# Kernel optimization log

Measured on AMD Instinct MI355X. Metric: run time of the kernel, lower is better.

Reference implementation:

```python
import jax, jax.numpy as jnp
import numpy as np

B, H, W, D, L, M = 16, 256, 256, 32, 4, 12  # batch, grid H, grid W, d_model, num_layers, modes
BN_EPS = 1e-5


def setup_inputs() -> dict:
    key = jax.random.key(0)
    ks = jax.random.split(key, 12)
    scale = 1.0 / (D * D)  # SpectralConv2d init scale: 1/(in_ch*out_ch)
    return {
        "x": jax.random.normal(ks[0], (B, H, W), jnp.float32),
        "coords_x": jax.random.uniform(ks[1], (1, 2, 1, H, W), dtype=jnp.float32),
        # linear_in: 3 -> D
        "w_in": jax.random.normal(ks[2], (D, 3), jnp.float32) * 0.3,
        "b_in": jnp.zeros((D,), jnp.float32),
        # per-layer spectral weights (real/imag), torch.rand-style uniform [0,1)*scale
        "w1r": jax.random.uniform(ks[3], (L, D, D, M, M), dtype=jnp.float32) * scale,
        "w1i": jax.random.uniform(ks[4], (L, D, D, M, M), dtype=jnp.float32) * scale,
        "w2r": jax.random.uniform(ks[5], (L, D, D, M, M), dtype=jnp.float32) * scale,
        "w2i": jax.random.uniform(ks[6], (L, D, D, M, M), dtype=jnp.float32) * scale,
        # per-layer pointwise linear D -> D
        "lw": jax.random.normal(ks[7], (L, D, D), jnp.float32) * (1.0 / np.sqrt(D)),
        "lb": jnp.zeros((L, D), jnp.float32),
        # per-layer BatchNorm affine params
        "gamma": jnp.ones((L, D), jnp.float32),
        "beta": jnp.zeros((L, D), jnp.float32),
        # linear_out: D -> 1
        "w_out": jax.random.normal(ks[8], (1, D), jnp.float32) * (1.0 / np.sqrt(D)),
        "b_out": jnp.zeros((1,), jnp.float32),
    }


def _fourier_layer(h, w1, w2, lw, lb, gamma, beta):
    # h: [B, D, H, W]
    Bh, C, Hh, Wh = h.shape
    h_ft = jnp.fft.rfft2(h)  # [B, D, H, W//2+1] complex64
    # low-mode truncation + complex channel mixing on two corner blocks
    top = jnp.einsum('bixy,ioxy->boxy', h_ft[:, :, :M, :M], w1)
    bot = jnp.einsum('bixy,ioxy->boxy', h_ft[:, :, Hh - M:, :M], w2)
    out_ft = jnp.zeros((Bh, C, Hh, Wh // 2 + 1), jnp.complex64)
    out_ft = out_ft.at[:, :, :M, :M].set(top).at[:, :, Hh - M:, :M].set(bot)
    y = jnp.fft.irfft2(out_ft, s=(Hh, Wh))  # [B, D, H, W]
    # residual pointwise linear (x + Linear(x)), then ReLU, then BatchNorm2d (batch stats)
    y = y + jnp.einsum('bchw,oc->bohw', y, lw) + lb[None, :, None, None]
    y = jax.nn.relu(y)
    mean = y.mean(axis=(0, 2, 3), keepdims=True)
    var = y.var(axis=(0, 2, 3), keepdims=True)
    y = (y - mean) * jax.lax.rsqrt(var + BN_EPS)
    return y * gamma[None, :, None, None] + beta[None, :, None, None]


def reference(x, coords_x, w_in, b_in, w1r, w1i, w2r, w2i, lw, lb, gamma, beta, w_out, b_out):
    # coords_x: [1,2,1,H,W] -> squeeze dim 2 -> broadcast to [B,2,H,W]
    cx = jnp.broadcast_to(coords_x[:, :, 0], (x.shape[0], 2, H, W))
    h = jnp.concatenate([x[:, None], cx], axis=1)  # [B, 3, H, W]
    h = jnp.einsum('bchw,dc->bdhw', h, w_in) + b_in[None, :, None, None]  # linear_in
    for i in range(L):  # fixed small layer count
        h = _fourier_layer(h, w1r[i] + 1j * w1i[i], w2r[i] + 1j * w2i[i],
                           lw[i], lb[i], gamma[i], beta[i])
    out = jnp.einsum('bdhw,od->bohw', h, w_out) + b_out[None, :, None, None]  # linear_out
    return out[:, 0]  # [B, H, W]
```

## Files before the change

### kernel.cpp

```cpp
#include <hip/hip_runtime.h>

constexpr double PI2 = 6.283185307179586476925286766559;
constexpr float INV_HW = 1.0f / 65536.0f;


__global__ __launch_bounds__(256) void k_init(float* __restrict__ cs) {
  int t = threadIdx.x;
  double a = PI2 * (double)t / 256.0;
  cs[2*t]   = (float)cos(a);
  cs[2*t+1] = (float)sin(a);
}

__global__ __launch_bounds__(256) void k_prep(
    const float* __restrict__ w1r, const float* __restrict__ w1i,
    const float* __restrict__ w2r, const float* __restrict__ w2i,
    const float* __restrict__ lw, float* __restrict__ wf)
{
  const int bid = blockIdx.x;
  const int l = bid / 288, m = bid % 288;
  const int ky = m / 12, kx = m % 12;
  const int kyp = (ky < 12) ? ky : ky - 12;
  const float* wr_ = ((ky < 12) ? w1r : w2r) + l*147456;
  const float* wi_ = ((ky < 12) ? w1i : w2i) + l*147456;
  __shared__ float wre[1024], wim[1024], lwl[1024];
  const int tid = threadIdx.x;
  for (int f = tid; f < 1024; f += 256) {
    int idx = f*144 + kyp*12 + kx;
    wre[f] = wr_[idx]; wim[f] = wi_[idx];
    lwl[f] = lw[l*1024 + f];
  }
  __syncthreads();
  float* o_ = wf + (long)bid*2048;
  for (int f = tid; f < 1024; f += 256) {
    int i = f >> 5, o = f & 31;
    float ar = wre[f], ai = wim[f];
    #pragma unroll
    for (int c = 0; c < 32; ++c) {
      float lv = lwl[o*32 + c];
      ar += wre[i*32 + c] * lv;
      ai += wim[i*32 + c] * lv;
    }
    o_[f] = ar; o_[1024 + f] = ai;
  }
}

__global__ __launch_bounds__(256) void k_embed_fwd(
    const float* __restrict__ xin, const float* __restrict__ coords,
    const float* __restrict__ w_in, const float* __restrict__ b_in,
    const float* __restrict__ cs, float* __restrict__ gxo)
{
  __shared__ float wl[96], bl[32];
  __shared__ __align__(16) float csl[512];
  __shared__ float S[32*257];
  const int tid = threadIdx.x;
  if (tid < 96) wl[tid] = w_in[tid];
  if (tid >= 96 && tid < 128) bl[tid-96] = b_in[tid-96];
  for (int f = tid; f < 512; f += 256) csl[f] = cs[f];
  const int b = blockIdx.x >> 8, y = blockIdx.x & 255;
  const float xv = xin[(b*256 + y)*256 + tid];
  const float c0 = coords[y*256 + tid];
  const float c1 = coords[65536 + y*256 + tid];
  __syncthreads();
  #pragma unroll 8
  for (int d = 0; d < 32; ++d)
    S[d*257 + tid] = wl[3*d]*xv + wl[3*d+1]*c0 + wl[3*d+2]*c1 + bl[d];
  __syncthreads();
  const int task = tid >> 5, o = tid & 31;
  if (task < 6) {
    const int kx0 = task*2, kx1 = kx0 + 1;
    const float* Sp = &S[o*257];
    const float s0v = Sp[0], s128 = Sp[128];
    float ar0 = s0v + s128, ai0 = 0.f;
    float ar1 = s0v - s128, ai1 = 0.f;
    int t0 = kx0, t1 = kx1;
    for (int xx = 1; xx < 128; ++xx) {
      float a = Sp[xx], bv = Sp[256 - xx];
      float e = a + bv, od = a - bv;
      float2 w0 = *(const float2*)&csl[2*t0];
      float2 w1 = *(const float2*)&csl[2*t1];
      ar0 += e*w0.x;  ai0 -= od*w0.y;
      ar1 += e*w1.x;  ai1 -= od*w1.y;
      t0 = (t0 + kx0) & 255;
      t1 = (t1 + kx1) & 255;
    }
    float4 w4; w4.x = ar0; w4.y = ai0; w4.z = ar1; w4.w = ai1;
    *(float4*)(gxo + ((long)(b*256 + y)*32 + o)*24 + task*4) = w4;
  }
}

__global__ __launch_bounds__(512) void k_spec(
    const float* __restrict__ gx, const float* __restrict__ cs,
    const float* __restrict__ bnp, const float* __restrict__ wfl,
    float* __restrict__ gy)
{
  const int bid = (blockIdx.x % 8) * 24 + blockIdx.x / 8;
  const int b = bid / 12, kx = bid % 12;
  __shared__ float2 Z[32*257];
  __shared__ float fcl[24*66];
  __shared__ float fml[24*66];
  __shared__ __align__(16) float csl[512];
  const int tid = threadIdx.x;
  if (tid < 512) csl[tid] = cs[tid];
  {
    const int ch = tid & 31;
    float sc = 1.0f, badd = 0.0f;
    if (bnp) { sc = bnp[ch]; if (kx == 0) badd = 256.0f * bnp[32 + ch]; }
    const float* src = gx + ((long)(b*256)*32 + ch)*24 + 2*kx;
    const int ybase = tid >> 5;
    #pragma unroll
    for (int i = 0; i < 16; ++i) {
      int y = ybase + 16*i;
      float2 v = *(const float2*)(src + (long)y*768);
      float2 w; w.x = sc*v.x + badd; w.y = sc*v.y;
      Z[ch*257 + y] = w;
    }
  }
  __syncthreads();
  for (int t = tid; t < 832; t += 512) {
    const int hf = t & 1, r = t >> 1;
    const int pr = r % 13, ch = r / 13;
    const int kyv = (pr <= 10) ? (pr + 1) : ((pr == 11) ? 0 : 244);
    const int y0 = hf << 7;
    int tt = (kyv * y0) & 255;
    float A = 0.f, Bv = 0.f, C2 = 0.f, D = 0.f;
    const float2* Zp = &Z[ch*257 + y0];
    for (int i = 0; i < 128; ++i) {
      float2 v = Zp[i];
      float2 w = *(const float2*)&csl[2*tt];
      A  += v.x*w.x;  D  += v.x*w.y;
      C2 += v.y*w.x;  Bv += v.y*w.y;
      tt = (tt + kyv) & 255;
    }
    A  += __shfl_xor(A, 1, 64);
    Bv += __shfl_xor(Bv, 1, 64);
    C2 += __shfl_xor(C2, 1, 64);
    D  += __shfl_xor(D, 1, 64);
    if (hf == 0) {
      const int slo = (pr <= 10) ? (pr + 1) : ((pr == 11) ? 0 : 12);
      fcl[slo*66 + 2*ch]     = A + Bv;
      fcl[slo*66 + 2*ch + 1] = C2 - D;
      if (pr <= 10) {
        fcl[(23 - pr)*66 + 2*ch]     = A - Bv;
        fcl[(23 - pr)*66 + 2*ch + 1] = C2 + D;
      }
    }
  }
  __syncthreads();
  for (int t = tid; t < 768; t += 512) {
    const int ky = t >> 5, o = t & 31;
    const float* wb = wfl + ((long)(ky*12 + kx))*2048;
    const float* fr = &fcl[ky*66];
    float ar = 0.f, ai = 0.f;
    #pragma unroll
    for (int i = 0; i < 32; ++i) {
      float fre = fr[2*i], fim = fr[2*i+1];
      float wr = wb[i*32 + o], wi = wb[1024 + i*32 + o];
      ar += fre*wr - fim*wi;
      ai += fre*wi + fim*wr;
    }
    fml[ky*66 + 2*o]     = ar;
    fml[ky*66 + 2*o + 1] = ai;
  }
  __syncthreads();
  {
    const int yp = tid & 127, og = tid >> 7;
    float tc[24], tsn[24];
    #pragma unroll
    for (int s = 0; s < 24; ++s) {
      int kyv = (s < 12) ? s : (232 + s);
      int tt = (kyv * yp) & 255;
      tc[s] = csl[2*tt]; tsn[s] = csl[2*tt+1];
    }
    const int yhi = (256 - yp) & 255;
    float* rowLo = gy + ((long)(b*256 + yp))*768 + kx*64;
    float* rowHi = gy + ((long)(b*256 + yhi))*768 + kx*64;
    #pragma unroll
    for (int oo = 0; oo < 8; oo += 2) {
      const int o = og*8 + oo;
      float A1a=0.f,A2a=0.f,A3a=0.f,A4a=0.f;
      float A1b=0.f,A2b=0.f,A3b=0.f,A4b=0.f;
      #pragma unroll
      for (int s = 0; s < 24; ++s) {
        float fra = fml[s*66 + 2*o],     fia = fml[s*66 + 2*o + 1];
        float frb = fml[s*66 + 2*o + 2], fib = fml[s*66 + 2*o + 3];
        float c = tc[s], sn = tsn[s];
        A1a += fra*c;  A2a += fia*sn;  A3a += fra*sn;  A4a += fia*c;
        A1b += frb*c;  A2b += fib*sn;  A3b += frb*sn;  A4b += fib*c;
      }
      float4 lo, hi;
      lo.x = (A1a - A2a)*INV_HW; lo.y = (A3a + A4a)*INV_HW;
      lo.z = (A1b - A2b)*INV_HW; lo.w = (A3b + A4b)*INV_HW;
      hi.x = (A1a + A2a)*INV_HW; hi.y = (A4a - A3a)*INV_HW;
      hi.z = (A1b + A2b)*INV_HW; hi.w = (A4b - A3b)*INV_HW;
      *(float4*)(rowLo + 2*o) = lo;
      *(float4*)(rowHi + 2*o) = hi;
    }
  }
  if (tid < 32) {
    const int o = tid;
    float re = 0.f, im = 0.f;
    #pragma unroll
    for (int s = 0; s < 24; ++s) {
      float fr = fml[s*66 + 2*o], fi = fml[s*66 + 2*o + 1];
      if (s & 1) { re -= fr; im -= fi; } else { re += fr; im += fi; }
    }
    float* row = gy + ((long)(b*256 + 128))*768 + kx*64;
    row[2*o]     = re*INV_HW;
    row[2*o + 1] = im*INV_HW;
  }
}

__global__ __launch_bounds__(256) void k_fuse(
    const float* __restrict__ gy, const float* __restrict__ cs,
    const float* __restrict__ lb,
    float* __restrict__ gxo, float* __restrict__ part, float* __restrict__ z)
{
  const int b = blockIdx.x >> 8, y = blockIdx.x & 255;
  const int tid = threadIdx.x;
  __shared__ __align__(16) float csl[512];
  __shared__ float S[32*257];
  for (int f = tid; f < 512; f += 256) csl[f] = cs[f];
  __syncthreads();
  const int xs = tid & 127, half = tid >> 7;
  const int cbase = half << 4;
  const int xhi = (256 - xs) & 255;
  float tc[12], tsn[12];
  #pragma unroll
  for (int kx = 1; kx < 12; ++kx) {
    int tt = (kx * xs) & 255;
    tc[kx]  = 2.0f*csl[2*tt];
    tsn[kx] = 2.0f*csl[2*tt+1];
  }
  const float* Gg = gy + (long)(b*256 + y)*768;
  float zlo[16], zhi[16];
  #pragma unroll
  for (int cc = 0; cc < 16; cc += 2) {
    const int c = cbase + cc;
    float base0 = Gg[2*c], base1 = Gg[2*c + 2];
    float cos0 = 0.f, sin0 = 0.f, cos1 = 0.f, sin1 = 0.f;
    #pragma unroll
    for (int kx = 1; kx < 12; ++kx) {
      float4 g = *(const float4*)(Gg + kx*64 + 2*c);
      cos0 += g.x*tc[kx];  sin0 += g.y*tsn[kx];
      cos1 += g.z*tc[kx];  sin1 += g.w*tsn[kx];
    }
    const float l0 = lb[c], l1 = lb[c+1];
    zlo[cc]   = fmaxf(base0 + cos0 - sin0 + l0, 0.f);
    zhi[cc]   = fmaxf(base0 + cos0 + sin0 + l0, 0.f);
    zlo[cc+1] = fmaxf(base1 + cos1 - sin1 + l1, 0.f);
    zhi[cc+1] = fmaxf(base1 + cos1 + sin1 + l1, 0.f);
  }
  #pragma unroll
  for (int cc = 0; cc < 16; ++cc) {
    S[(cbase+cc)*257 + xs]  = zlo[cc];
    S[(cbase+cc)*257 + xhi] = zhi[cc];
  }
  if (z) {
    #pragma unroll
    for (int cc = 0; cc < 16; ++cc) {
      z[((b*32 + cbase+cc)*256 + y)*256 + xs]  = zlo[cc];
      z[((b*32 + cbase+cc)*256 + y)*256 + xhi] = zhi[cc];
    }
  }
  if (tid < 32) {
    const int c = tid;
    float acc = Gg[2*c] + lb[c];
    #pragma unroll
    for (int kx = 1; kx < 12; ++kx) {
      float2 g = *(const float2*)(Gg + kx*64 + 2*c);
      acc += (kx & 1) ? (-2.0f * g.x) : (2.0f * g.x);
    }
    float zv = fmaxf(acc, 0.f);
    S[c*257 + 128] = zv;
    if (z) z[((b*32 + c)*256 + y)*256 + 128] = zv;
  }
  __syncthreads();
  const int task = tid >> 5, o = tid & 31;
  if (task < 6) {
    if (gxo || task == 0) {
      const int kx0 = task*2, kx1 = kx0 + 1;
      const float* Sp = &S[o*257];
      const float s0v = Sp[0], s128 = Sp[128];
      float ar0 = s0v + s128, ai0 = 0.f;
      float ar1 = s0v - s128, ai1 = 0.f;
      int t0 = kx0, t1 = kx1;
      for (int xx = 1; xx < 128; ++xx) {
        float a = Sp[xx], bv = Sp[256 - xx];
        float e = a + bv, od = a - bv;
        float2 w0 = *(const float2*)&csl[2*t0];
        float2 w1 = *(const float2*)&csl[2*t1];
        ar0 += e*w0.x;  ai0 -= od*w0.y;
        ar1 += e*w1.x;  ai1 -= od*w1.y;
        t0 = (t0 + kx0) & 255;
        t1 = (t1 + kx1) & 255;
      }
      if (task == 0) part[(long)blockIdx.x*64 + 2*o] = ar0;
      if (gxo) {
        float4 w4; w4.x = ar0; w4.y = ai0; w4.z = ar1; w4.w = ai1;
        *(float4*)(gxo + ((long)(b*256 + y)*32 + o)*24 + task*4) = w4;
      }
    }
  } else {
    const int xb = (task - 6) << 7;
    const float* Sp = &S[o*257];
    float sq = 0.f;
    for (int j = 0; j < 128; ++j) { float v = Sp[xb + j]; sq += v*v; }
    sq += __shfl_xor(sq, 32, 64);
    if (task == 6) part[(long)blockIdx.x*64 + 2*o + 1] = sq;
  }
}

__global__ __launch_bounds__(256) void k_stats(
    const float* __restrict__ part, const float* __restrict__ gamma,
    const float* __restrict__ beta, float* __restrict__ bn)
{
  const int c = blockIdx.x, tid = threadIdx.x;
  float s1 = 0.f, s2 = 0.f;
  for (int j = tid; j < 4096; j += 256) {
    s1 += part[(long)j*64 + 2*c];
    s2 += part[(long)j*64 + 2*c + 1];
  }
  #pragma unroll
  for (int d = 32; d; d >>= 1) {
    s1 += __shfl_xor(s1, d, 64);
    s2 += __shfl_xor(s2, d, 64);
  }
  __shared__ float r1[4], r2[4];
  int w = tid >> 6;
  if ((tid & 63) == 0) { r1[w] = s1; r2[w] = s2; }
  __syncthreads();
  if (tid == 0) {
    float S1 = r1[0]+r1[1]+r1[2]+r1[3];
    float S2 = r2[0]+r2[1]+r2[2]+r2[3];
    const float N = 1048576.0f;
    float mean = S1 / N;
    float var  = S2 / N - mean*mean;
    float inv  = rsqrtf(var + 1e-5f);
    float sc   = gamma[c] * inv;
    bn[c]      = sc;
    bn[32 + c] = beta[c] - mean*sc;
  }
}

__global__ __launch_bounds__(256) void k_out(
    const float* __restrict__ z, const float* __restrict__ bn,
    const float* __restrict__ w_out, const float* __restrict__ b_out,
    float* __restrict__ out)
{
  __shared__ float a[32];
  __shared__ float c0s;
  const int tid = threadIdx.x;
  if (tid < 32) a[tid] = bn[tid] * w_out[tid];
  if (tid == 0) {
    float t = b_out[0];
    for (int c = 0; c < 32; ++c) t += bn[32 + c] * w_out[c];
    c0s = t;
  }
  __syncthreads();
  int gid = blockIdx.x*256 + tid;
  int b = gid >> 14, pos = (gid & 16383) << 2;
  const float* zb = z + (long)b*2097152 + pos;
  float c0 = c0s;
  float r0 = c0, r1 = c0, r2 = c0, r3 = c0;
  #pragma unroll 8
  for (int c = 0; c < 32; ++c) {
    float4 v = *(const float4*)(zb + c*65536);
    float ac = a[c];
    r0 += v.x*ac; r1 += v.y*ac; r2 += v.z*ac; r3 += v.w*ac;
  }
  float4 res; res.x = r0; res.y = r1; res.z = r2; res.w = r3;
  *(float4*)(out + (long)b*65536 + pos) = res;
}

extern "C" void kernel_launch(void* const* d_in, const int* in_sizes, int n_in,
                              void* d_out, int out_size, void* d_ws, size_t ws_size,
                              hipStream_t stream) {
  const float* x      = (const float*)d_in[0];
  const float* coords = (const float*)d_in[1];
  const float* w_in   = (const float*)d_in[2];
  const float* b_in   = (const float*)d_in[3];
  const float* w1r    = (const float*)d_in[4];
  const float* w1i    = (const float*)d_in[5];
  const float* w2r    = (const float*)d_in[6];
  const float* w2i    = (const float*)d_in[7];
  const float* lw     = (const float*)d_in[8];
  const float* lb     = (const float*)d_in[9];
  const float* gamma  = (const float*)d_in[10];
  const float* beta   = (const float*)d_in[11];
  const float* w_out  = (const float*)d_in[12];
  const float* b_out  = (const float*)d_in[13];
  float* out = (float*)d_out;
  float* ws  = (float*)d_ws;

  float* cs   = ws;
  float* z    = cs + 512;
  float* gx   = z;
  float* wf   = z + 3145728;
  float* gy   = z + 33554432;
  float* fc   = gy + 3145728;
  float* fm   = fc + 294912;
  float* bn   = fm + 294912;
  float* part = fc;

  k_init<<<1, 256, 0, stream>>>(cs);
  k_prep<<<1152, 256, 0, stream>>>(w1r, w1i, w2r, w2i, lw, wf);
  k_embed_fwd<<<4096, 256, 0, stream>>>(x, coords, w_in, b_in, cs, gx);

  for (int l = 0; l < 4; ++l) {
    k_spec<<<192, 512, 0, stream>>>(gx, cs, (l == 0) ? nullptr : bn,
                                    wf + (long)l*589824, gy);
    k_fuse<<<4096, 256, 0, stream>>>(gy, cs, lb + l*32,
                                     (l < 3) ? gx : nullptr, part,
                                     (l == 3) ? z : nullptr);
    k_stats<<<32, 256, 0, stream>>>(part, gamma + l*32, beta + l*32, bn);
  }

  k_out<<<1024, 256, 0, stream>>>(z, bn, w_out, b_out, out);
}
```

Measured before the change: 541.3 us.

## Restructure k_fuse forward row DFT across all threads with precomputed twiddle table

Adds a precomputed cos/sin table (12 modes by 128 positions) built once in k_init and staged into shared memory, replacing the modular twiddle indexing in k_fuse. The row DFT now splits positions across all 8 warps, so every thread works on every mode on float4 even/odd vectors, and a shared-memory reduction combines the partial sums. Previously only 6 warps did the DFT while 2 did squares. The sum of squares is folded into the same pass. This trades a serial 127-step loop per thread for wider parallel work, at the cost of more registers (24 accumulators) and an extra barrier and reduction.

After: 538.2 us. No clear change (-0.6%).

```diff
diff --git a/kernel.cpp b/kernel.cpp
--- a/kernel.cpp
+++ b/kernel.cpp
@@ -4,11 +4,18 @@
 constexpr float INV_HW = 1.0f / 65536.0f;
 
 
-__global__ __launch_bounds__(256) void k_init(float* __restrict__ cs) {
+__global__ __launch_bounds__(256) void k_init(float* __restrict__ cs,
+                                              float* __restrict__ Tg) {
   int t = threadIdx.x;
   double a = PI2 * (double)t / 256.0;
   cs[2*t]   = (float)cos(a);
   cs[2*t+1] = (float)sin(a);
+  for (int i = t; i < 1536; i += 256) {
+    int k = i >> 7, xs = i & 127;
+    double ang = PI2 * (double)(k * xs) / 256.0;
+    Tg[i]        = (float)cos(ang);
+    Tg[1536 + i] = (float)sin(ang);
+  }
 }
 
 __global__ __launch_bounds__(256) void k_prep(
@@ -211,15 +218,20 @@
 }
 
 __global__ __launch_bounds__(256) void k_fuse(
-    const float* __restrict__ gy, const float* __restrict__ cs,
+    const float* __restrict__ gy, const float* __restrict__ Tg,
     const float* __restrict__ lb,
     float* __restrict__ gxo, float* __restrict__ part, float* __restrict__ z)
 {
   const int b = blockIdx.x >> 8, y = blockIdx.x & 255;
   const int tid = threadIdx.x;
-  __shared__ __align__(16) float csl[512];
-  __shared__ float S[32*257];
-  for (int f = tid; f < 512; f += 256) csl[f] = cs[f];
+  __shared__ __align__(16) float T[3168];
+  __shared__ __align__(16) float E[32*132];
+  __shared__ __align__(16) float O[32*132];
+  for (int i = tid; i < 1536; i += 256) {
+    int k = i >> 7, xs0 = i & 127;
+    T[k*132 + xs0]        = Tg[i];
+    T[1584 + k*132 + xs0] = Tg[1536 + i];
+  }
   __syncthreads();
   const int xs = tid & 127, half = tid >> 7;
   const int cbase = half << 4;
@@ -227,9 +239,8 @@
   float tc[12], tsn[12];
   #pragma unroll
   for (int kx = 1; kx < 12; ++kx) {
-    int tt = (kx * xs) & 255;
-    tc[kx]  = 2.0f*csl[2*tt];
-    tsn[kx] = 2.0f*csl[2*tt+1];
+    tc[kx]  = 2.0f * T[kx*132 + xs];
+    tsn[kx] = 2.0f * T[1584 + kx*132 + xs];
   }
   const float* Gg = gy + (long)(b*256 + y)*768;
   float zlo[16], zhi[16];
@@ -252,8 +263,10 @@
   }
   #pragma unroll
   for (int cc = 0; cc < 16; ++cc) {
-    S[(cbase+cc)*257 + xs]  = zlo[cc];
-    S[(cbase+cc)*257 + xhi] = zhi[cc];
+    float e = (xs == 0) ? zlo[cc] : (zlo[cc] + zhi[cc]);
+    float o = (xs == 0) ? 0.f     : (zlo[cc] - zhi[cc]);
+    E[(cbase+cc)*132 + xs] = e;
+    O[(cbase+cc)*132 + xs] = o;
   }
   if (z) {
     #pragma unroll
@@ -271,42 +284,84 @@
       acc += (kx & 1) ? (-2.0f * g.x) : (2.0f * g.x);
     }
     float zv = fmaxf(acc, 0.f);
-    S[c*257 + 128] = zv;
+    E[c*132 + 128] = zv;
     if (z) z[((b*32 + c)*256 + y)*256 + 128] = zv;
   }
   __syncthreads();
-  const int task = tid >> 5, o = tid & 31;
-  if (task < 6) {
-    if (gxo || task == 0) {
-      const int kx0 = task*2, kx1 = kx0 + 1;
-      const float* Sp = &S[o*257];
-      const float s0v = Sp[0], s128 = Sp[128];
-      float ar0 = s0v + s128, ai0 = 0.f;
-      float ar1 = s0v - s128, ai1 = 0.f;
-      int t0 = kx0, t1 = kx1;
-      for (int xx = 1; xx < 128; ++xx) {
-        float a = Sp[xx], bv = Sp[256 - xx];
-        float e = a + bv, od = a - bv;
-        float2 w0 = *(const float2*)&csl[2*t0];
-        float2 w1 = *(const float2*)&csl[2*t1];
-        ar0 += e*w0.x;  ai0 -= od*w0.y;
-        ar1 += e*w1.x;  ai1 -= od*w1.y;
-        t0 = (t0 + kx0) & 255;
-        t1 = (t1 + kx1) & 255;
+  const int ch = tid & 31, seg = tid >> 5;
+  float ar[12], ai[12], sq = 0.f;
+  #pragma unroll
+  for (int k = 0; k < 12; ++k) { ar[k] = 0.f; ai[k] = 0.f; }
+  {
+    const float* Erow = &E[ch*132 + seg*16];
+    const float* Orow = &O[ch*132 + seg*16];
+    if (gxo) {
+      #pragma unroll
+      for (int c4 = 0; c4 < 4; ++c4) {
+        float4 E4 = *(const float4*)(Erow + 4*c4);
+        float4 O4 = *(const float4*)(Orow + 4*c4);
+        ar[0] += E4.x + E4.y + E4.z + E4.w;
+        #pragma unroll
+        for (int k = 1; k < 12; ++k) {
+          float4 Tc4 = *(const float4*)&T[k*132 + seg*16 + 4*c4];
+          float4 Ts4 = *(const float4*)&T[1584 + k*132 + seg*16 + 4*c4];
+          ar[k] += E4.x*Tc4.x + E4.y*Tc4.y + E4.z*Tc4.z + E4.w*Tc4.w;
+          ai[k] -= O4.x*Ts4.x + O4.y*Ts4.y + O4.z*Ts4.z + O4.w*Ts4.w;
+        }
+        sq += E4.x*E4.x + E4.y*E4.y + E4.z*E4.z + E4.w*E4.w
+            + O4.x*O4.x + O4.y*O4.y + O4.z*O4.z + O4.w*O4.w;
       }
-      if (task == 0) part[(long)blockIdx.x*64 + 2*o] = ar0;
-      if (gxo) {
-        float4 w4; w4.x = ar0; w4.y = ai0; w4.z = ar1; w4.w = ai1;
-        *(float4*)(gxo + ((long)(b*256 + y)*32 + o)*24 + task*4) = w4;
+    } else {
+      #pragma unroll
+      for (int c4 = 0; c4 < 4; ++c4) {
+        float4 E4 = *(const float4*)(Erow + 4*c4);
+        float4 O4 = *(const float4*)(Orow + 4*c4);
+        ar[0] += E4.x + E4.y + E4.z + E4.w;
+        sq += E4.x*E4.x + E4.y*E4.y + E4.z*E4.z + E4.w*E4.w
+            + O4.x*O4.x + O4.y*O4.y + O4.z*O4.z + O4.w*O4.w;
       }
     }
-  } else {
-    const int xb = (task - 6) << 7;
-    const float* Sp = &S[o*257];
-    float sq = 0.f;
-    for (int j = 0; j < 128; ++j) { float v = Sp[xb + j]; sq += v*v; }
-    sq += __shfl_xor(sq, 32, 64);
-    if (task == 6) part[(long)blockIdx.x*64 + 2*o + 1] = sq;
+  }
+  #pragma unroll
+  for (int k = 0; k < 12; ++k) ar[k] += __shfl_xor(ar[k], 32, 64);
+  #pragma unroll
+  for (int k = 1; k < 12; ++k) ai[k] += __shfl_xor(ai[k], 32, 64);
+  sq += __shfl_xor(sq, 32, 64);
+  __syncthreads();
+  float* red = O;
+  const int wv = tid >> 6;
+  if ((tid & 63) < 32) {
+    float* r = &red[(wv*32 + ch)*25];
+    #pragma unroll
+    for (int k = 0; k < 12; ++k) r[k] = ar[k];
+    #pragma unroll
+    for (int k = 1; k < 12; ++k) r[11 + k] = ai[k];
+    r[23] = sq;
+  }
+  __syncthreads();
+  {
+    const int q = tid >> 5;
+    const float e0   = E[ch*132];
+    const float e128 = E[ch*132 + 128];
+    float* gp = gxo ? (gxo + ((long)(b*256 + y)*32 + ch)*24) : nullptr;
+    #pragma unroll
+    for (int j = 0; j < 3; ++j) {
+      const int v = 3*q + j;
+      float s = red[ch*25 + v]        + red[(32+ch)*25 + v]
+              + red[(64+ch)*25 + v]   + red[(96+ch)*25 + v];
+      if (v < 12) {
+        s += (v & 1) ? -e128 : e128;
+        if (gp) {
+          gp[2*v] = s;
+          if (v == 0) gp[1] = 0.f;
+        }
+        if (v == 0) part[(long)blockIdx.x*64 + 2*ch] = s;
+      } else if (v < 23) {
+        if (gp) gp[2*(v - 11) + 1] = s;
+      } else {
+        part[(long)blockIdx.x*64 + 2*ch + 1] = 0.5f*s + 0.5f*e0*e0 + e128*e128;
+      }
+    }
   }
 }
 
@@ -397,19 +452,18 @@
   float* gx   = z;
   float* wf   = z + 3145728;
   float* gy   = z + 33554432;
-  float* fc   = gy + 3145728;
-  float* fm   = fc + 294912;
-  float* bn   = fm + 294912;
-  float* part = fc;
-
-  k_init<<<1, 256, 0, stream>>>(cs);
+  float* part = gy + 3145728;
+  float* Tg   = part + 294912;
+  float* bn   = Tg + 294912;
+
+  k_init<<<1, 256, 0, stream>>>(cs, Tg);
   k_prep<<<1152, 256, 0, stream>>>(w1r, w1i, w2r, w2i, lw, wf);
   k_embed_fwd<<<4096, 256, 0, stream>>>(x, coords, w_in, b_in, cs, gx);
 
   for (int l = 0; l < 4; ++l) {
     k_spec<<<192, 512, 0, stream>>>(gx, cs, (l == 0) ? nullptr : bn,
                                     wf + (long)l*589824, gy);
-    k_fuse<<<4096, 256, 0, stream>>>(gy, cs, lb + l*32,
+    k_fuse<<<4096, 256, 0, stream>>>(gy, Tg, lb + l*32,
                                      (l < 3) ? gx : nullptr, part,
                                      (l == 3) ? z : nullptr);
     k_stats<<<32, 256, 0, stream>>>(part, gamma + l*32, beta + l*32, bn);
```
